# Performance work log

Measured on AMD Instinct MI355X. Metric: run time of the kernel, lower is better.

## Reference

```python
import jax, jax.numpy as jnp
import numpy as np
from jax import lax

SIGMA = 1.0
ALPHA = 1.0
BETA = 1.0
TRUNCATE = 4.0  # scipy.ndimage default


def _gauss_kernel(sigma):
    radius = int(TRUNCATE * sigma + 0.5)  # scipy radius rule -> 4 for sigma=1
    x = np.arange(-radius, radius + 1, dtype=np.float64)
    k = np.exp(-0.5 * (x / sigma) ** 2)
    k = (k / k.sum()).astype(np.float32)
    return k

_KERNEL = _gauss_kernel(SIGMA)


def _blur_axis(img, k, axis):
    # scipy mode='reflect' == jnp.pad mode='symmetric' (edge repeated)
    r = len(k) // 2
    pad = [(0, 0)] * img.ndim
    pad[axis] = (r, r)
    xp = jnp.pad(img, pad, mode='symmetric')
    n = img.shape[axis]
    out = k[0] * lax.slice_in_dim(xp, 0, n, axis=axis)
    for i in range(1, len(k)):
        out = out + k[i] * lax.slice_in_dim(xp, i, i + n, axis=axis)
    return out


def gaussian_blur(img):
    # scalar sigma in scipy blurs along EVERY axis, including batch & channel
    k = jnp.asarray(_KERNEL, dtype=img.dtype)
    for ax in range(img.ndim):
        img = _blur_axis(img, k, ax)
    return img


def decompose(I):
    I_log = jnp.log(I + 1e-6)
    I_smooth = gaussian_blur(I_log)
    R = I_log - I_smooth
    L = I_log - R  # == I_smooth
    return jnp.exp(L), jnp.exp(R)


def setup_inputs() -> dict:
    key = jax.random.key(0)
    k1, k2 = jax.random.split(key)
    shape = (16, 3, 512, 512)
    I_enhanced = jax.random.uniform(k1, shape, dtype=jnp.float32)
    I_gt = jax.random.uniform(k2, shape, dtype=jnp.float32)
    return {"I_enhanced": I_enhanced, "I_gt": I_gt}


def reference(I_enhanced, I_gt):
    L_enh, R_enh = decompose(I_enhanced)
    L_gt, R_gt = decompose(I_gt)
    L_reflectance = jnp.mean((R_enh - R_gt) ** 2)
    L_illumination = jnp.mean((L_enh - L_gt) ** 2)
    return ALPHA * L_reflectance + BETA * L_illumination
```

## Files before the change

kernel.cpp:

```cpp
#include <hip/hip_runtime.h>
#include <cmath>

#define PLANE (512*512)
#define NPLANES 48
#define NEL (48*PLANE)

struct Taps { float k[9]; };
struct CMat { float w[3][3]; };


__global__ __launch_bounds__(64)
void k_blur_hw(const float* __restrict__ inE, const float* __restrict__ inG,
               float* __restrict__ ws, Taps tp)
{
    const int l  = threadIdx.x;
    const int r0 = blockIdx.x * 32;
    const int z  = blockIdx.y;

    const float* src = (z < NPLANES) ? (inE + z * PLANE)
                                     : (inG + (z - NPLANES) * PLANE);

    const bool is0  = (l == 0);
    const bool is63 = (l == 63);
    const int  vout = (l >> 3) * 6144 + (l & 7) * 8;

    float ring[10][8];

#define FOLD(r) ((r) < 0 ? (-1 - (r)) : ((r) > 511 ? (1023 - (r)) : (r)))

    float4 a, b, c, d, e, f;
    {
        int rr;
        rr = FOLD(r0 - 4);
        a = *(const float4*)(src + rr * 512 + l * 8);
        b = *(const float4*)(src + rr * 512 + l * 8 + 4);
        rr = FOLD(r0 - 3);
        c = *(const float4*)(src + rr * 512 + l * 8);
        d = *(const float4*)(src + rr * 512 + l * 8 + 4);
        rr = FOLD(r0 - 2);
        e = *(const float4*)(src + rr * 512 + l * 8);
        f = *(const float4*)(src + rr * 512 + l * 8 + 4);
    }

    for (int jb = 0; jb < 40; jb += 10) {
#pragma unroll
        for (int u = 0; u < 10; ++u) {
            const int j = jb + u;

            float win[16];
            win[4]  = __logf(a.x + 1e-6f);
            win[5]  = __logf(a.y + 1e-6f);
            win[6]  = __logf(a.z + 1e-6f);
            win[7]  = __logf(a.w + 1e-6f);
            win[8]  = __logf(b.x + 1e-6f);
            win[9]  = __logf(b.y + 1e-6f);
            win[10] = __logf(b.z + 1e-6f);
            win[11] = __logf(b.w + 1e-6f);

            a = c; b = d; c = e; d = f;
            if (j + 3 < 40) {
                int rn = FOLD(r0 - 4 + j + 3);
                const float* nrp = src + rn * 512 + l * 8;
                e = *(const float4*)nrp;
                f = *(const float4*)(nrp + 4);
            }

            float s;
            s = __shfl_up(win[8], 1);   win[0]  = is0  ? win[7]  : s;
            s = __shfl_up(win[9], 1);   win[1]  = is0  ? win[6]  : s;
            s = __shfl_up(win[10], 1);  win[2]  = is0  ? win[5]  : s;
            s = __shfl_up(win[11], 1);  win[3]  = is0  ? win[4]  : s;
            s = __shfl_down(win[4], 1); win[12] = is63 ? win[11] : s;
            s = __shfl_down(win[5], 1); win[13] = is63 ? win[10] : s;
            s = __shfl_down(win[6], 1); win[14] = is63 ? win[9]  : s;
            s = __shfl_down(win[7], 1); win[15] = is63 ? win[8]  : s;

#pragma unroll
            for (int i = 0; i < 8; ++i) {
                float o = 0.f;
#pragma unroll
                for (int t = 0; t < 9; ++t) o += tp.k[t] * win[i + t];
                ring[u][i] = o;
            }

            if (j >= 8) {
                float acc[8];
#pragma unroll
                for (int i = 0; i < 8; ++i) {
                    float o = 0.f;
#pragma unroll
                    for (int t = 0; t < 9; ++t)
                        o += tp.k[t] * ring[(u + 2 + t) % 10][i];
                    acc[i] = o;
                }
                const int ro = r0 + j - 8;
                float* dp = ws + (ro * 768 + z) * 64 + vout;
                *(float4*)dp       = make_float4(acc[0], acc[1], acc[2], acc[3]);
                *(float4*)(dp + 4) = make_float4(acc[4], acc[5], acc[6], acc[7]);
            }
        }
    }
#undef FOLD
}

__global__ __launch_bounds__(256)
void k_cn_loss(const float* __restrict__ ws, const float* __restrict__ Ie,
               const float* __restrict__ Ig, float* __restrict__ part,
               Taps tp, CMat cm)
{
    const int tid = threadIdx.x;
    const int hw  = blockIdx.x * 256 + tid;
    const float* wbase = ws + (hw >> 6) * (96 * 64) + (hw & 63);

    float re[9][3];
    float rg[9][3];

#define LOADRAW(m, vE, vG)                                                     \
    vE[0] = wbase[((m) * 3 + 0) * 64];                                         \
    vE[1] = wbase[((m) * 3 + 1) * 64];                                         \
    vE[2] = wbase[((m) * 3 + 2) * 64];                                         \
    vG[0] = wbase[(48 + (m) * 3 + 0) * 64];                                    \
    vG[1] = wbase[(48 + (m) * 3 + 1) * 64];                                    \
    vG[2] = wbase[(48 + (m) * 3 + 2) * 64];

#define CBLUR(v, dst)                                                          \
    dst[0] = cm.w[0][0] * v[0] + cm.w[0][1] * v[1] + cm.w[0][2] * v[2];        \
    dst[1] = cm.w[1][0] * v[0] + cm.w[1][1] * v[1] + cm.w[1][2] * v[2];        \
    dst[2] = cm.w[2][0] * v[0] + cm.w[2][1] * v[1] + cm.w[2][2] * v[2];

#pragma unroll
    for (int m = 0; m < 4; ++m) {
        float vE[3], vG[3];
        LOADRAW(m, vE, vG);
        CBLUR(vE, re[m]); CBLUR(vG, rg[m]);
    }
    float nvE[3], nvG[3];
    LOADRAW(4, nvE, nvG);
    float ieq[3], igq[3];
#pragma unroll
    for (int c = 0; c < 3; ++c) {
        ieq[c] = Ie[c * PLANE + hw] + 1e-6f;
        igq[c] = Ig[c * PLANE + hw] + 1e-6f;
    }

    float acc = 0.f;
#pragma unroll
    for (int n = 0; n < 16; ++n) {
        float nie[3], nig[3];
        if (n + 1 < 16) {
#pragma unroll
            for (int c = 0; c < 3; ++c) {
                nie[c] = Ie[((n + 1) * 3 + c) * PLANE + hw] + 1e-6f;
                nig[c] = Ig[((n + 1) * 3 + c) * PLANE + hw] + 1e-6f;
            }
        }
        const int mnew = n + 4;
        if (mnew < 16) {
            CBLUR(nvE, re[mnew % 9]); CBLUR(nvG, rg[mnew % 9]);
            if (mnew + 1 < 16) { LOADRAW(mnew + 1, nvE, nvG); }
        }
#pragma unroll
        for (int c = 0; c < 3; ++c) {
            float se = 0.f, sg = 0.f;
#pragma unroll
            for (int t = 0; t < 9; ++t) {
                int m = n - 4 + t;
                m = (m < 0) ? (-1 - m) : ((m > 15) ? (31 - m) : m);
                se += tp.k[t] * re[m % 9][c];
                sg += tp.k[t] * rg[m % 9][c];
            }
            float ee = __expf(-se);
            float eg = __expf(-sg);
            float Re = ieq[c] * ee;
            float Rg = igq[c] * eg;
            float Le = __builtin_amdgcn_rcpf(ee);
            float Lg = __builtin_amdgcn_rcpf(eg);
            float dr = Re - Rg;
            float dl = Le - Lg;
            acc += dr * dr + dl * dl;
        }
        if (n + 1 < 16) {
#pragma unroll
            for (int c = 0; c < 3; ++c) { ieq[c] = nie[c]; igq[c] = nig[c]; }
        }
    }
#undef LOADRAW
#undef CBLUR

    __shared__ float red[256];
    red[tid] = acc;
    __syncthreads();
#pragma unroll
    for (int s = 128; s > 0; s >>= 1) {
        if (tid < s) red[tid] += red[tid + s];
        __syncthreads();
    }
    if (tid == 0) part[blockIdx.x] = red[0];
}

__global__ __launch_bounds__(256)
void k_final(const float* __restrict__ part, float* __restrict__ out)
{
    __shared__ float red[256];
    float a = 0.f;
    for (int i = threadIdx.x; i < 1024; i += 256) a += part[i];
    red[threadIdx.x] = a;
    __syncthreads();
#pragma unroll
    for (int s = 128; s > 0; s >>= 1) {
        if (threadIdx.x < s) red[threadIdx.x] += red[threadIdx.x + s];
        __syncthreads();
    }
    if (threadIdx.x == 0) out[0] = red[0] * (1.0f / (float)NEL);
}

extern "C" void kernel_launch(void* const* d_in, const int* in_sizes, int n_in,
                              void* d_out, int out_size, void* d_ws, size_t ws_size,
                              hipStream_t stream) {
    const float* Ie = (const float*)d_in[0];
    const float* Ig = (const float*)d_in[1];

    Taps tp;
    {
        double kk[9], s = 0.0;
        for (int i = 0; i < 9; ++i) { double x = (double)(i - 4); kk[i] = exp(-0.5 * x * x); s += kk[i]; }
        for (int i = 0; i < 9; ++i) tp.k[i] = (float)(kk[i] / s);
    }

    CMat cm;
    {
        for (int c = 0; c < 3; ++c) {
            cm.w[c][0] = cm.w[c][1] = cm.w[c][2] = 0.f;
            for (int t = 0; t < 9; ++t) {
                int m = c - 4 + t;
                int mm = ((m % 6) + 6) % 6;
                if (mm > 2) mm = 5 - mm;
                cm.w[c][mm] += tp.k[t];
            }
        }
    }

    float* ws   = (float*)d_ws;
    float* part = ws + 2 * (size_t)NEL;

    dim3 g1(16, 96);
    k_blur_hw<<<g1, 64, 0, stream>>>(Ie, Ig, ws, tp);
    k_cn_loss<<<1024, 256, 0, stream>>>(ws, Ie, Ig, part, tp, cm);
    k_final<<<1, 256, 0, stream>>>(part, (float*)d_out);
}
```

Before: 184.1 us.

## Store blurred intermediate in fp16, split width across blocks, fuse final reduction via atomics

The intermediate buffer is stored as packed fp16 instead of fp32, halving workspace write and read traffic between the two passes. The row blur now splits each row into two 256-wide halves with halo loads, doubling block count and cutting per-thread registers. The final reduction kernel is removed in favour of a memset plus per-block atomicAdd into the output. fp16 storage of log-domain blurred values adds rounding error to the loss, and float atomics make the summation order nondeterministic.

```diff
diff --git a/kernel.cpp b/kernel.cpp
--- a/kernel.cpp
+++ b/kernel.cpp
@@ -1,4 +1,5 @@
 #include <hip/hip_runtime.h>
+#include <hip/hip_fp16.h>
 #include <cmath>
 
 #define PLANE (512*512)
@@ -11,35 +12,37 @@
 
 __global__ __launch_bounds__(64)
 void k_blur_hw(const float* __restrict__ inE, const float* __restrict__ inG,
-               float* __restrict__ ws, Taps tp)
+               ushort* __restrict__ ws, Taps tp)
 {
-    const int l  = threadIdx.x;
-    const int r0 = blockIdx.x * 32;
-    const int z  = blockIdx.y;
+    const int l    = threadIdx.x;
+    const int w0   = (blockIdx.x & 1) * 256;
+    const int r0   = (blockIdx.x >> 1) * 32;
+    const int z    = blockIdx.y;
 
     const float* src = (z < NPLANES) ? (inE + z * PLANE)
                                      : (inG + (z - NPLANES) * PLANE);
 
-    const bool is0  = (l == 0);
-    const bool is63 = (l == 63);
-    const int  vout = (l >> 3) * 6144 + (l & 7) * 8;
-
-    float ring[10][8];
+    const int  col   = w0 + 4 * l;
+    const bool is0   = (l == 0);
+    const bool is63  = (l == 63);
+    const bool ledge = (w0 == 0);
+    const bool redge = (w0 + 256 == 512);
+    const bool do_halo = (is0 && !ledge) || (is63 && !redge);
+    const int  hoff  = is0 ? (w0 - 4) : (w0 + 256);
+    const int  tile  = col >> 6;
+    const int  inner = col & 63;
+
+    float ring[10][4];
 
 #define FOLD(r) ((r) < 0 ? (-1 - (r)) : ((r) > 511 ? (1023 - (r)) : (r)))
 
-    float4 a, b, c, d, e, f;
-    {
-        int rr;
-        rr = FOLD(r0 - 4);
-        a = *(const float4*)(src + rr * 512 + l * 8);
-        b = *(const float4*)(src + rr * 512 + l * 8 + 4);
-        rr = FOLD(r0 - 3);
-        c = *(const float4*)(src + rr * 512 + l * 8);
-        d = *(const float4*)(src + rr * 512 + l * 8 + 4);
-        rr = FOLD(r0 - 2);
-        e = *(const float4*)(src + rr * 512 + l * 8);
-        f = *(const float4*)(src + rr * 512 + l * 8 + 4);
+    float4 pown[3], phal[3];
+    phal[0] = phal[1] = phal[2] = make_float4(1.f, 1.f, 1.f, 1.f);
+#pragma unroll
+    for (int s = 0; s < 3; ++s) {
+        const float* rp = src + FOLD(r0 - 4 + s) * 512;
+        pown[s] = *(const float4*)(rp + col);
+        if (do_halo) phal[s] = *(const float4*)(rp + hoff);
     }
 
     for (int jb = 0; jb < 40; jb += 10) {
@@ -47,36 +50,45 @@
         for (int u = 0; u < 10; ++u) {
             const int j = jb + u;
 
-            float win[16];
-            win[4]  = __logf(a.x + 1e-6f);
-            win[5]  = __logf(a.y + 1e-6f);
-            win[6]  = __logf(a.z + 1e-6f);
-            win[7]  = __logf(a.w + 1e-6f);
-            win[8]  = __logf(b.x + 1e-6f);
-            win[9]  = __logf(b.y + 1e-6f);
-            win[10] = __logf(b.z + 1e-6f);
-            win[11] = __logf(b.w + 1e-6f);
-
-            a = c; b = d; c = e; d = f;
+            float4 own = pown[0], hal = phal[0];
+            pown[0] = pown[1]; pown[1] = pown[2];
+            phal[0] = phal[1]; phal[1] = phal[2];
             if (j + 3 < 40) {
-                int rn = FOLD(r0 - 4 + j + 3);
-                const float* nrp = src + rn * 512 + l * 8;
-                e = *(const float4*)nrp;
-                f = *(const float4*)(nrp + 4);
-            }
-
-            float s;
-            s = __shfl_up(win[8], 1);   win[0]  = is0  ? win[7]  : s;
-            s = __shfl_up(win[9], 1);   win[1]  = is0  ? win[6]  : s;
-            s = __shfl_up(win[10], 1);  win[2]  = is0  ? win[5]  : s;
-            s = __shfl_up(win[11], 1);  win[3]  = is0  ? win[4]  : s;
-            s = __shfl_down(win[4], 1); win[12] = is63 ? win[11] : s;
-            s = __shfl_down(win[5], 1); win[13] = is63 ? win[10] : s;
-            s = __shfl_down(win[6], 1); win[14] = is63 ? win[9]  : s;
-            s = __shfl_down(win[7], 1); win[15] = is63 ? win[8]  : s;
-
-#pragma unroll
-            for (int i = 0; i < 8; ++i) {
+                const float* rp = src + FOLD(r0 - 1 + j) * 512;
+                pown[2] = *(const float4*)(rp + col);
+                if (do_halo) phal[2] = *(const float4*)(rp + hoff);
+            }
+
+            const float w4 = __logf(own.x + 1e-6f);
+            const float w5 = __logf(own.y + 1e-6f);
+            const float w6 = __logf(own.z + 1e-6f);
+            const float w7 = __logf(own.w + 1e-6f);
+            const float h0 = __logf(hal.x + 1e-6f);
+            const float h1 = __logf(hal.y + 1e-6f);
+            const float h2 = __logf(hal.z + 1e-6f);
+            const float h3 = __logf(hal.w + 1e-6f);
+
+            float win[12];
+            win[4] = w4; win[5] = w5; win[6] = w6; win[7] = w7;
+            win[0] = __shfl_up(w4, 1);
+            win[1] = __shfl_up(w5, 1);
+            win[2] = __shfl_up(w6, 1);
+            win[3] = __shfl_up(w7, 1);
+            win[8]  = __shfl_down(w4, 1);
+            win[9]  = __shfl_down(w5, 1);
+            win[10] = __shfl_down(w6, 1);
+            win[11] = __shfl_down(w7, 1);
+            if (is0) {
+                if (ledge) { win[0] = w7; win[1] = w6; win[2] = w5; win[3] = w4; }
+                else       { win[0] = h0; win[1] = h1; win[2] = h2; win[3] = h3; }
+            }
+            if (is63) {
+                if (redge) { win[8] = w7; win[9] = w6; win[10] = w5; win[11] = w4; }
+                else       { win[8] = h0; win[9] = h1; win[10] = h2; win[11] = h3; }
+            }
+
+#pragma unroll
+            for (int i = 0; i < 4; ++i) {
                 float o = 0.f;
 #pragma unroll
                 for (int t = 0; t < 9; ++t) o += tp.k[t] * win[i + t];
@@ -84,9 +96,9 @@
             }
 
             if (j >= 8) {
-                float acc[8];
-#pragma unroll
-                for (int i = 0; i < 8; ++i) {
+                float acc[4];
+#pragma unroll
+                for (int i = 0; i < 4; ++i) {
                     float o = 0.f;
 #pragma unroll
                     for (int t = 0; t < 9; ++t)
@@ -94,9 +106,11 @@
                     acc[i] = o;
                 }
                 const int ro = r0 + j - 8;
-                float* dp = ws + (ro * 768 + z) * 64 + vout;
-                *(float4*)dp       = make_float4(acc[0], acc[1], acc[2], acc[3]);
-                *(float4*)(dp + 4) = make_float4(acc[4], acc[5], acc[6], acc[7]);
+                __half2 pa, pb;
+                pa.x = __float2half(acc[0]); pa.y = __float2half(acc[1]);
+                pb.x = __float2half(acc[2]); pb.y = __float2half(acc[3]);
+                ushort* dp = ws + (((ro * 8 + tile) * 96) + z) * 64 + inner;
+                *(uint2*)dp = make_uint2(*(uint*)&pa, *(uint*)&pb);
             }
         }
     }
@@ -104,24 +118,24 @@
 }
 
 __global__ __launch_bounds__(256)
-void k_cn_loss(const float* __restrict__ ws, const float* __restrict__ Ie,
-               const float* __restrict__ Ig, float* __restrict__ part,
+void k_cn_loss(const __half* __restrict__ ws, const float* __restrict__ Ie,
+               const float* __restrict__ Ig, float* __restrict__ out,
                Taps tp, CMat cm)
 {
     const int tid = threadIdx.x;
     const int hw  = blockIdx.x * 256 + tid;
-    const float* wbase = ws + (hw >> 6) * (96 * 64) + (hw & 63);
+    const __half* wbase = ws + (hw >> 6) * (96 * 64) + (hw & 63);
 
     float re[9][3];
     float rg[9][3];
 
 #define LOADRAW(m, vE, vG)                                                     \
-    vE[0] = wbase[((m) * 3 + 0) * 64];                                         \
-    vE[1] = wbase[((m) * 3 + 1) * 64];                                         \
-    vE[2] = wbase[((m) * 3 + 2) * 64];                                         \
-    vG[0] = wbase[(48 + (m) * 3 + 0) * 64];                                    \
-    vG[1] = wbase[(48 + (m) * 3 + 1) * 64];                                    \
-    vG[2] = wbase[(48 + (m) * 3 + 2) * 64];
+    vE[0] = __half2float(wbase[((m) * 3 + 0) * 64]);                           \
+    vE[1] = __half2float(wbase[((m) * 3 + 1) * 64]);                           \
+    vE[2] = __half2float(wbase[((m) * 3 + 2) * 64]);                           \
+    vG[0] = __half2float(wbase[(48 + (m) * 3 + 0) * 64]);                      \
+    vG[1] = __half2float(wbase[(48 + (m) * 3 + 1) * 64]);                      \
+    vG[2] = __half2float(wbase[(48 + (m) * 3 + 2) * 64]);
 
 #define CBLUR(v, dst)                                                          \
     dst[0] = cm.w[0][0] * v[0] + cm.w[0][1] * v[1] + cm.w[0][2] * v[2];        \
@@ -195,23 +209,7 @@
         if (tid < s) red[tid] += red[tid + s];
         __syncthreads();
     }
-    if (tid == 0) part[blockIdx.x] = red[0];
-}
-
-__global__ __launch_bounds__(256)
-void k_final(const float* __restrict__ part, float* __restrict__ out)
-{
-    __shared__ float red[256];
-    float a = 0.f;
-    for (int i = threadIdx.x; i < 1024; i += 256) a += part[i];
-    red[threadIdx.x] = a;
-    __syncthreads();
-#pragma unroll
-    for (int s = 128; s > 0; s >>= 1) {
-        if (threadIdx.x < s) red[threadIdx.x] += red[threadIdx.x + s];
-        __syncthreads();
-    }
-    if (threadIdx.x == 0) out[0] = red[0] * (1.0f / (float)NEL);
+    if (tid == 0) atomicAdd(out, red[0] * (1.0f / (float)NEL));
 }
 
 extern "C" void kernel_launch(void* const* d_in, const int* in_sizes, int n_in,
@@ -240,11 +238,11 @@
         }
     }
 
-    float* ws   = (float*)d_ws;
-    float* part = ws + 2 * (size_t)NEL;
-
-    dim3 g1(16, 96);
+    ushort* ws = (ushort*)d_ws;
+
+    hipMemsetAsync(d_out, 0, sizeof(float), stream);
+    dim3 g1(32, 96);
     k_blur_hw<<<g1, 64, 0, stream>>>(Ie, Ig, ws, tp);
-    k_cn_loss<<<1024, 256, 0, stream>>>(ws, Ie, Ig, part, tp, cm);
-    k_final<<<1, 256, 0, stream>>>(part, (float*)d_out);
+    k_cn_loss<<<1024, 256, 0, stream>>>((const __half*)ws, Ie, Ig,
+                                        (float*)d_out, tp, cm);
 }
```

Measured after the change: 183.2 us. Within noise of the previous version (-0.5%).
